# Optimization experiments

Measured on AMD Instinct MI355X. Metric: run time of the kernel, lower is better.

The kernel has to match this reference:

```python
import jax, jax.numpy as jnp
import numpy as np

D_MODEL = 1024
NUM_HEADS = 16
D_K = D_MODEL // NUM_HEADS
THETA = 10000.0
BATCH = 2
SEQ = 2048


def _trunc_normal(key, shape, std):
    # approximate trunc_normal init; exact init distribution is irrelevant for correctness
    return jnp.clip(jax.random.normal(key, shape) * std, -3.0 * std, 3.0 * std)


def setup_inputs() -> dict:
    key = jax.random.key(0)
    ks = jax.random.split(key, 6)
    std = np.sqrt(2.0 / (D_MODEL + D_MODEL)).astype(np.float32)
    x = jax.random.normal(ks[0], (BATCH, SEQ, D_MODEL), dtype=jnp.float32)
    token_positions = jnp.tile(jnp.arange(SEQ, dtype=jnp.int32), (BATCH, 1))
    wq = _trunc_normal(ks[1], (D_MODEL, D_MODEL), std)  # (out, in)
    wk = _trunc_normal(ks[2], (D_MODEL, D_MODEL), std)
    wv = _trunc_normal(ks[3], (D_MODEL, D_MODEL), std)
    wo = _trunc_normal(ks[4], (D_MODEL, D_MODEL), std)
    return {"in_features": x, "wq": wq, "wk": wk, "wv": wv, "wo": wo,
            "token_positions": token_positions}


def _apply_rope(x, token_positions):
    # x: (B, H, S, d_k); token_positions: (B, S)
    half = D_K // 2
    inv_freq = 1.0 / (THETA ** (2.0 * jnp.arange(half, dtype=jnp.float32) / D_K))
    ang = token_positions.astype(jnp.float32)[..., None] * inv_freq  # (B, S, half)
    cos = jnp.cos(ang)[:, None, :, :]  # (B, 1, S, half) broadcast over heads
    sin = jnp.sin(ang)[:, None, :, :]
    x_even = x[..., 0::2]
    x_odd = x[..., 1::2]
    rot_even = x_even * cos - x_odd * sin
    rot_odd = x_even * sin + x_odd * cos
    return jnp.stack([rot_even, rot_odd], axis=-1).reshape(x.shape)


def reference(in_features, wq, wk, wv, wo, token_positions):
    B, S, _ = in_features.shape
    # bias-free linear: weight is (out, in)
    q = jnp.einsum('bsi,oi->bso', in_features, wq)
    k = jnp.einsum('bsi,oi->bso', in_features, wk)
    v = jnp.einsum('bsi,oi->bso', in_features, wv)
    # split heads: (B, H, S, d_k)
    def split(t):
        return t.reshape(B, S, NUM_HEADS, D_K).transpose(0, 2, 1, 3)
    qh, kh, vh = split(q), split(k), split(v)
    qh = _apply_rope(qh, token_positions)
    kh = _apply_rope(kh, token_positions)
    scale = 1.0 / jnp.sqrt(jnp.float32(D_K))
    logits = jnp.einsum('bhqd,bhkd->bhqk', qh, kh) * scale  # (B, H, S, S)
    causal = jnp.tril(jnp.ones((S, S), dtype=bool))
    logits = jnp.where(causal, logits, -jnp.inf)
    weights = jax.nn.softmax(logits, axis=-1)
    out = jnp.einsum('bhqk,bhkd->bhqd', weights, vh)  # (B, H, S, d_k)
    out = out.transpose(0, 2, 1, 3).reshape(B, S, D_MODEL)
    return jnp.einsum('bsi,oi->bso', out, wo)
```

## Files before the change

kernel.cpp:

```cpp
#include <hip/hip_runtime.h>
#include <hip/hip_bf16.h>
#include <math.h>

#define D_MODEL 1024
#define NUM_HEADS 16
#define DK 64
#define BATCH 2
#define SEQ 2048
#define NROWS (BATCH * SEQ)

typedef __bf16 bf16x8 __attribute__((ext_vector_type(8)));
typedef __bf16 bf16x4 __attribute__((ext_vector_type(4)));
typedef float f32x4 __attribute__((ext_vector_type(4)));

#define GLOAD_LDS16(g, l)                                          \
  __builtin_amdgcn_global_load_lds(                                \
      (const __attribute__((address_space(1))) void*)(g),          \
      (__attribute__((address_space(3))) void*)(l), 16, 0, 0)

#define LDS_FENCE() asm volatile("s_waitcnt lgkmcnt(0)" ::: "memory")

__global__ void cvt_all_kernel(const float* __restrict__ x,
                               const float* __restrict__ wq,
                               const float* __restrict__ wk,
                               const float* __restrict__ wv,
                               const float* __restrict__ wo,
                               __hip_bfloat16* __restrict__ xb,
                               __hip_bfloat16* __restrict__ wqkvb,
                               __hip_bfloat16* __restrict__ wob) {
  int t = blockIdx.x * 256 + threadIdx.x;
  const float* src;
  __hip_bfloat16* dst;
  int off;
  if (t < 1048576) {
    src = x; dst = xb; off = t;
  } else {
    int u = t - 1048576;
    int w = u >> 18;
    off = u & 262143;
    src = (w == 0) ? wq : (w == 1) ? wk : (w == 2) ? wv : wo;
    dst = (w < 3) ? (wqkvb + (size_t)w * 1048576) : wob;
  }
  float4 v = reinterpret_cast<const float4*>(src)[off];
  union { __hip_bfloat16 h[4]; uint2 u; } tmp;
  tmp.h[0] = __float2bfloat16(v.x);
  tmp.h[1] = __float2bfloat16(v.y);
  tmp.h[2] = __float2bfloat16(v.z);
  tmp.h[3] = __float2bfloat16(v.w);
  reinterpret_cast<uint2*>(dst)[off] = tmp.u;
}

__global__ __launch_bounds__(256)
void gemm_qkv_kernel(const __hip_bfloat16* __restrict__ A,
                     const __hip_bfloat16* __restrict__ W,
                     __hip_bfloat16* __restrict__ O0,
                     __hip_bfloat16* __restrict__ O1,
                     __hip_bfloat16* __restrict__ Vt) {
  __shared__ __hip_bfloat16 smem[2][2][128 * 32];
#define sAg(b) (smem[0][b])
#define sBg(b) (smem[1][b])
  const int tid = threadIdx.x;
  const int wave = tid >> 6, lane = tid & 63, quad = lane >> 4, l16 = lane & 15;
  const int wm = (wave >> 1) * 64, wn = (wave & 1) * 64;
  const int bm = blockIdx.x * 128;
  const int bnG = blockIdx.y * 128;
  const int which = blockIdx.y >> 3;
  const int ocol = bnG & 1023;
  const int srow = lane >> 2, scol = (lane & 3) * 8;

#pragma unroll
  for (int c = 0; c < 2; ++c) {
    int ch = wave + c * 4;
    GLOAD_LDS16(&A[(size_t)(bm + ch * 16 + srow) * D_MODEL + scol], &sAg(0)[ch * 512]);
    GLOAD_LDS16(&W[(size_t)(bnG + ch * 16 + srow) * D_MODEL + scol], &sBg(0)[ch * 512]);
  }

  f32x4 acc[4][4] = {};
  for (int it = 0; it < 32; ++it) {
    __syncthreads();
    if (it + 1 < 32) {
      const int k0 = (it + 1) * 32, nb = (it + 1) & 1;
#pragma unroll
      for (int c = 0; c < 2; ++c) {
        int ch = wave + c * 4;
        GLOAD_LDS16(&A[(size_t)(bm + ch * 16 + srow) * D_MODEL + k0 + scol],
                    &sAg(nb)[ch * 512]);
        GLOAD_LDS16(&W[(size_t)(bnG + ch * 16 + srow) * D_MODEL + k0 + scol],
                    &sBg(nb)[ch * 512]);
      }
    }
    const int cb = it & 1;
    bf16x8 af[4], bfb[4];
#pragma unroll
    for (int i = 0; i < 4; ++i)
      af[i] = *reinterpret_cast<bf16x8*>(&sAg(cb)[(wm + i * 16 + l16) * 32 + quad * 8]);
#pragma unroll
    for (int j = 0; j < 4; ++j)
      bfb[j] = *reinterpret_cast<bf16x8*>(&sBg(cb)[(wn + j * 16 + l16) * 32 + quad * 8]);
#pragma unroll
    for (int i = 0; i < 4; ++i)
#pragma unroll
      for (int j = 0; j < 4; ++j)
        acc[i][j] = __builtin_amdgcn_mfma_f32_16x16x32_bf16(af[i], bfb[j], acc[i][j], 0, 0, 0);
  }

  if (which < 2) {
    __hip_bfloat16* O = (which == 0) ? O0 : O1;
#pragma unroll
    for (int i = 0; i < 4; ++i)
#pragma unroll
      for (int j = 0; j < 4; ++j)
#pragma unroll
        for (int r = 0; r < 4; ++r) {
          int row = bm + wm + i * 16 + quad * 4 + r;
          int col = ocol + wn + j * 16 + l16;
          O[(size_t)row * D_MODEL + col] = __float2bfloat16(acc[i][j][r]);
        }
  } else {
    __syncthreads();
    __hip_bfloat16* tr = &smem[0][0][0];
#pragma unroll
    for (int i = 0; i < 4; ++i)
#pragma unroll
      for (int j = 0; j < 4; ++j) {
        int c = wn + j * 16 + l16;
        int r = wm + i * 16 + quad * 4;
        bf16x4 pk;
#pragma unroll
        for (int rr = 0; rr < 4; ++rr) pk[rr] = (__bf16)acc[i][j][rr];
        int g = (r >> 3) ^ (c & 15);
        *reinterpret_cast<bf16x4*>(&tr[c * 128 + g * 8 + (r & 7)]) = pk;
      }
    __syncthreads();
    int c = tid >> 1;
    int vcol = ocol + c;
    int hh = vcol >> 6, dd = vcol & 63;
    int bb = bm >> 11, s0 = (bm & 2047) + (tid & 1) * 64;
    __hip_bfloat16* dst = Vt + ((size_t)(bb * 16 + hh) * 64 + dd) * 2048 + s0;
    int gbase = (tid & 1) * 8;
#pragma unroll
    for (int k = 0; k < 8; ++k) {
      int g = (gbase + k) ^ (c & 15);
      *reinterpret_cast<bf16x8*>(&dst[k * 8]) =
          *reinterpret_cast<bf16x8*>(&tr[c * 128 + g * 8]);
    }
  }
#undef sAg
#undef sBg
}

__global__ __launch_bounds__(256)
void gemm_out_kernel(const __hip_bfloat16* __restrict__ A,
                     const __hip_bfloat16* __restrict__ W,
                     float* __restrict__ O) {
  __shared__ __hip_bfloat16 sA[2][64 * 32];
  __shared__ __hip_bfloat16 sB[2][128 * 32];
  const int tid = threadIdx.x;
  const int wave = tid >> 6, lane = tid & 63, quad = lane >> 4, l16 = lane & 15;
  const int mh = (wave >> 1) * 32, nh = (wave & 1) * 64;
  const int bm = blockIdx.x * 64, bn = blockIdx.y * 128;
  const int srow = lane >> 2, scol = (lane & 3) * 8;

  GLOAD_LDS16(&A[(size_t)(bm + wave * 16 + srow) * D_MODEL + scol], &sA[0][wave * 512]);
#pragma unroll
  for (int c = 0; c < 2; ++c) {
    int ch = wave + c * 4;
    GLOAD_LDS16(&W[(size_t)(bn + ch * 16 + srow) * D_MODEL + scol], &sB[0][ch * 512]);
  }

  f32x4 acc[2][4] = {};
  for (int it = 0; it < 32; ++it) {
    __syncthreads();
    if (it + 1 < 32) {
      const int k0 = (it + 1) * 32, nb = (it + 1) & 1;
      GLOAD_LDS16(&A[(size_t)(bm + wave * 16 + srow) * D_MODEL + k0 + scol],
                  &sA[nb][wave * 512]);
#pragma unroll
      for (int c = 0; c < 2; ++c) {
        int ch = wave + c * 4;
        GLOAD_LDS16(&W[(size_t)(bn + ch * 16 + srow) * D_MODEL + k0 + scol],
                    &sB[nb][ch * 512]);
      }
    }
    const int cb = it & 1;
    bf16x8 af[2], bfb[4];
#pragma unroll
    for (int i = 0; i < 2; ++i)
      af[i] = *reinterpret_cast<bf16x8*>(&sA[cb][(mh + i * 16 + l16) * 32 + quad * 8]);
#pragma unroll
    for (int j = 0; j < 4; ++j)
      bfb[j] = *reinterpret_cast<bf16x8*>(&sB[cb][(nh + j * 16 + l16) * 32 + quad * 8]);
#pragma unroll
    for (int i = 0; i < 2; ++i)
#pragma unroll
      for (int j = 0; j < 4; ++j)
        acc[i][j] = __builtin_amdgcn_mfma_f32_16x16x32_bf16(af[i], bfb[j], acc[i][j], 0, 0, 0);
  }

#pragma unroll
  for (int i = 0; i < 2; ++i)
#pragma unroll
    for (int j = 0; j < 4; ++j)
#pragma unroll
      for (int r = 0; r < 4; ++r) {
        int row = bm + mh + i * 16 + quad * 4 + r;
        int col = bn + nh + j * 16 + l16;
        O[(size_t)row * D_MODEL + col] = acc[i][j][r];
      }
}

__global__ void rope_kernel(__hip_bfloat16* __restrict__ Q,
                            __hip_bfloat16* __restrict__ K,
                            const int* __restrict__ pos) {
  constexpr float QS = 0.18033688011112042f;
  int t = blockIdx.x * 256 + threadIdx.x;
  int row = t >> 7;
  int c = t & 127;
  int h = c >> 3, co = (c & 7) * 8;
  float ps = (float)pos[row];
  size_t off = (size_t)row * D_MODEL + h * DK + co;
  bf16x8 q = *reinterpret_cast<const bf16x8*>(&Q[off]);
  bf16x8 k = *reinterpret_cast<const bf16x8*>(&K[off]);
#pragma unroll
  for (int j = 0; j < 4; ++j) {
    float p = (float)((co >> 1) + j);
    float ang = ps * exp2f(-p * 0.41524101186091903f);
    float cs = cosf(ang), sn = sinf(ang);
    float qe = (float)q[2 * j], qo = (float)q[2 * j + 1];
    q[2 * j]     = (__bf16)((qe * cs - qo * sn) * QS);
    q[2 * j + 1] = (__bf16)((qe * sn + qo * cs) * QS);
    float ke = (float)k[2 * j], ko = (float)k[2 * j + 1];
    k[2 * j]     = (__bf16)(ke * cs - ko * sn);
    k[2 * j + 1] = (__bf16)(ke * sn + ko * cs);
  }
  *reinterpret_cast<bf16x8*>(&Q[off]) = q;
  *reinterpret_cast<bf16x8*>(&K[off]) = k;
}

__global__ __launch_bounds__(256)
void attn_kernel(const __hip_bfloat16* __restrict__ Q,
                 const __hip_bfloat16* __restrict__ K,
                 const __hip_bfloat16* __restrict__ Vt,
                 __hip_bfloat16* __restrict__ Ao) {
  __shared__ __hip_bfloat16 sK[2][64 * 64];
  __shared__ __hip_bfloat16 sVt[2][64 * 64];
  __shared__ __hip_bfloat16 sPt[4][16 * 64];
  const int tid = threadIdx.x;
  const int wave = tid >> 6, lane = tid & 63, quad = lane >> 4, l16 = lane & 15;
  const int idx = blockIdx.x;
  const int bh = idx & 31;
  const int half = (idx >> 5) & 1;
  const int pi = idx >> 6;
  const int qlo = pi, qhi = 15 - pi;
  const int h = bh & 15, b = bh >> 4;
  const int ho = h * DK;
  const size_t rowbase = (size_t)b * SEQ;
  const int jL = half * 4 + wave, jU = 7 - jL;
  const int sbs[2] = {qlo * 128 + jL * 16, qhi * 128 + jU * 16};
  const int nt = ((qhi * 128 + (7 - half * 4) * 16 + 15) >> 6) + 1;
  const __hip_bfloat16* Kbase = K + rowbase * D_MODEL + ho;
  const __hip_bfloat16* Vtbase = Vt + (size_t)(b * 16 + h) * 64 * 2048;

  bf16x8 aq[2][2];
#pragma unroll
  for (int s = 0; s < 2; ++s)
#pragma unroll
    for (int kk = 0; kk < 2; ++kk)
      aq[s][kk] = *reinterpret_cast<const bf16x8*>(
          &Q[(rowbase + sbs[s] + l16) * D_MODEL + ho + kk * 32 + quad * 8]);

  f32x4 o_acc[2][4] = {};
  float l_run[2] = {0.f, 0.f};

  const int srow = tid >> 2, sc = (tid & 3) * 16;
  const int ga = (tid & 3) * 2;
  const int sga = (ga ^ (srow & 7)) * 8, sgb = ((ga + 1) ^ (srow & 7)) * 8;

  {
    bf16x8 k0 = *reinterpret_cast<const bf16x8*>(&Kbase[(size_t)srow * D_MODEL + sc]);
    bf16x8 k1 = *reinterpret_cast<const bf16x8*>(&Kbase[(size_t)srow * D_MODEL + sc + 8]);
    bf16x8 v0 = *reinterpret_cast<const bf16x8*>(&Vtbase[(size_t)srow * 2048 + sc]);
    bf16x8 v1 = *reinterpret_cast<const bf16x8*>(&Vtbase[(size_t)srow * 2048 + sc + 8]);
    *reinterpret_cast<bf16x8*>(&sK[0][srow * 64 + sga]) = k0;
    *reinterpret_cast<bf16x8*>(&sK[0][srow * 64 + sgb]) = k1;
    *reinterpret_cast<bf16x8*>(&sVt[0][srow * 64 + sga]) = v0;
    *reinterpret_cast<bf16x8*>(&sVt[0][srow * 64 + sgb]) = v1;
  }

  for (int t = 0; t < nt; ++t) {
    __syncthreads();
    const int buf = t & 1;
    const bool hn = (t + 1) < nt;
    bf16x8 kn0, kn1, vn0, vn1;
    if (hn) {
      const int kvn = (t + 1) * 64;
      kn0 = *reinterpret_cast<const bf16x8*>(
          &Kbase[(size_t)(kvn + srow) * D_MODEL + sc]);
      kn1 = *reinterpret_cast<const bf16x8*>(
          &Kbase[(size_t)(kvn + srow) * D_MODEL + sc + 8]);
      vn0 = *reinterpret_cast<const bf16x8*>(
          &Vtbase[(size_t)srow * 2048 + kvn + sc]);
      vn1 = *reinterpret_cast<const bf16x8*>(
          &Vtbase[(size_t)srow * 2048 + kvn + sc + 8]);
    }

    const int kv0 = t * 64;
    if (kv0 <= sbs[1] + 15) {
      bf16x8 ak[2][4], bv[2][4];
#pragma unroll
      for (int kk = 0; kk < 2; ++kk)
#pragma unroll
        for (int j = 0; j < 4; ++j) {
          int go = ((4 * kk + quad) ^ (l16 & 7)) * 8;
          ak[kk][j] = *reinterpret_cast<bf16x8*>(&sK[buf][(j * 16 + l16) * 64 + go]);
          bv[kk][j] = *reinterpret_cast<bf16x8*>(&sVt[buf][(j * 16 + l16) * 64 + go]);
        }

#pragma unroll
      for (int s = 0; s < 2; ++s) {
        const int sb = sbs[s];
        if (kv0 > sb + 15) continue;
        f32x4 sv[4] = {};
#pragma unroll
        for (int kk = 0; kk < 2; ++kk)
#pragma unroll
          for (int j = 0; j < 4; ++j)
            sv[j] = __builtin_amdgcn_mfma_f32_16x16x32_bf16(ak[kk][j], aq[s][kk],
                                                            sv[j], 0, 0, 0);
        if (kv0 + 63 > sb) {
#pragma unroll
          for (int j = 0; j < 4; ++j)
#pragma unroll
            for (int r = 0; r < 4; ++r)
              if (kv0 + j * 16 + quad * 4 + r > sb + l16) sv[j][r] = -INFINITY;
        }
        float ls = 0.f;
#pragma unroll
        for (int j = 0; j < 4; ++j) {
          bf16x4 pk;
#pragma unroll
          for (int r = 0; r < 4; ++r) {
            float p = __builtin_amdgcn_exp2f(sv[j][r]);
            ls += p;
            pk[r] = (__bf16)p;
          }
          int wgr = (2 * j + (quad >> 1)) ^ (l16 & 7);
          *reinterpret_cast<bf16x4*>(
              &sPt[wave][l16 * 64 + wgr * 8 + (quad & 1) * 4]) = pk;
        }
        l_run[s] += ls;
        LDS_FENCE();
#pragma unroll
        for (int kk = 0; kk < 2; ++kk) {
          int rgr = (4 * kk + quad) ^ (l16 & 7);
          bf16x8 ap = *reinterpret_cast<bf16x8*>(&sPt[wave][l16 * 64 + rgr * 8]);
#pragma unroll
          for (int jd = 0; jd < 4; ++jd)
            o_acc[s][jd] = __builtin_amdgcn_mfma_f32_16x16x32_bf16(
                ap, bv[kk][jd], o_acc[s][jd], 0, 0, 0);
        }
      }
    }

    if (hn) {
      const int nb = buf ^ 1;
      *reinterpret_cast<bf16x8*>(&sK[nb][srow * 64 + sga]) = kn0;
      *reinterpret_cast<bf16x8*>(&sK[nb][srow * 64 + sgb]) = kn1;
      *reinterpret_cast<bf16x8*>(&sVt[nb][srow * 64 + sga]) = vn0;
      *reinterpret_cast<bf16x8*>(&sVt[nb][srow * 64 + sgb]) = vn1;
    }
  }

#pragma unroll
  for (int s = 0; s < 2; ++s) {
    float l = l_run[s];
    l += __shfl_xor(l, 16);
    l += __shfl_xor(l, 32);
    __hip_bfloat16* Aobase = Ao + (rowbase + sbs[s]) * D_MODEL + ho;
#pragma unroll
    for (int r = 0; r < 4; ++r) {
      float linv = 1.0f / __shfl(l, quad * 4 + r);
#pragma unroll
      for (int jd = 0; jd < 4; ++jd)
        Aobase[(size_t)(quad * 4 + r) * D_MODEL + jd * 16 + l16] =
            __float2bfloat16(o_acc[s][jd][r] * linv);
    }
  }
}

extern "C" void kernel_launch(void* const* d_in, const int* in_sizes, int n_in,
                              void* d_out, int out_size, void* d_ws, size_t ws_size,
                              hipStream_t stream) {
  const float* x = (const float*)d_in[0];
  const float* wq = (const float*)d_in[1];
  const float* wk = (const float*)d_in[2];
  const float* wv = (const float*)d_in[3];
  const float* wo = (const float*)d_in[4];
  const int* tpos = (const int*)d_in[5];
  float* out = (float*)d_out;
  char* ws = (char*)d_ws;

  __hip_bfloat16* xb    = (__hip_bfloat16*)(ws);
  __hip_bfloat16* wqkvb = (__hip_bfloat16*)(ws + (size_t)(8)  * 1048576);
  __hip_bfloat16* wob   = (__hip_bfloat16*)(ws + (size_t)(14) * 1048576);
  __hip_bfloat16* Qb    = (__hip_bfloat16*)(ws + (size_t)(16) * 1048576);
  __hip_bfloat16* Kb    = (__hip_bfloat16*)(ws + (size_t)(24) * 1048576);
  __hip_bfloat16* Vtb   = (__hip_bfloat16*)(ws + (size_t)(32) * 1048576);
  __hip_bfloat16* Aob   = xb;

  cvt_all_kernel<<<8192, 256, 0, stream>>>(x, wq, wk, wv, wo, xb, wqkvb, wob);

  gemm_qkv_kernel<<<dim3(32, 24), 256, 0, stream>>>(xb, wqkvb, Qb, Kb, Vtb);

  rope_kernel<<<2048, 256, 0, stream>>>(Qb, Kb, tpos);

  attn_kernel<<<512, 256, 0, stream>>>(Qb, Kb, Vtb, Aob);

  gemm_out_kernel<<<dim3(64, 8), 256, 0, stream>>>(Aob, wob, out);
}
```

Baseline: 182.4 us.

## Fuse RoPE into QKV GEMM epilogue and shrink output GEMM tiles

Applies the rotary embedding and the Q scaling directly in the QKV GEMM epilogue, pairing even and odd columns with a lane shuffle and using fast sincos. This removes the separate rope kernel launch and its full read-modify-write pass over Q and K. The output projection GEMM also switches from 64x128 to 64x64 tiles, doubling the grid to 1024 blocks for better CU occupancy at the cost of more redundant A loads. __sincosf is less accurate than cosf/sinf at the large angles produced by positions up to 2047.

```diff
diff --git a/kernel.cpp b/kernel.cpp
--- a/kernel.cpp
+++ b/kernel.cpp
@@ -53,9 +53,11 @@
 __global__ __launch_bounds__(256)
 void gemm_qkv_kernel(const __hip_bfloat16* __restrict__ A,
                      const __hip_bfloat16* __restrict__ W,
+                     const int* __restrict__ tpos,
                      __hip_bfloat16* __restrict__ O0,
                      __hip_bfloat16* __restrict__ O1,
                      __hip_bfloat16* __restrict__ Vt) {
+  constexpr float QS = 0.18033688011112042f;
   __shared__ __hip_bfloat16 smem[2][2][128 * 32];
 #define sAg(b) (smem[0][b])
 #define sBg(b) (smem[1][b])
@@ -106,16 +108,31 @@
 
   if (which < 2) {
     __hip_bfloat16* O = (which == 0) ? O0 : O1;
+    const float scale = (which == 0) ? QS : 1.0f;
+    const float sgn = (l16 & 1) ? 1.0f : -1.0f;
+    float invf[4];
+#pragma unroll
+    for (int j = 0; j < 4; ++j) {
+      int p = ((ocol + wn + j * 16 + l16) & 63) >> 1;
+      invf[j] = exp2f(-(float)p * 0.41524101186091903f);
+    }
 #pragma unroll
     for (int i = 0; i < 4; ++i)
 #pragma unroll
-      for (int j = 0; j < 4; ++j)
-#pragma unroll
-        for (int r = 0; r < 4; ++r) {
-          int row = bm + wm + i * 16 + quad * 4 + r;
+      for (int r = 0; r < 4; ++r) {
+        int row = bm + wm + i * 16 + quad * 4 + r;
+        float pos = (float)tpos[row];
+#pragma unroll
+        for (int j = 0; j < 4; ++j) {
+          float v = acc[i][j][r];
+          float partner = __shfl_xor(v, 1);
+          float sn, cs;
+          __sincosf(pos * invf[j], &sn, &cs);
+          float rot = (v * cs + sgn * partner * sn) * scale;
           int col = ocol + wn + j * 16 + l16;
-          O[(size_t)row * D_MODEL + col] = __float2bfloat16(acc[i][j][r]);
-        }
+          O[(size_t)row * D_MODEL + col] = __float2bfloat16(rot);
+        }
+      }
   } else {
     __syncthreads();
     __hip_bfloat16* tr = &smem[0][0][0];
@@ -154,87 +171,51 @@
                      const __hip_bfloat16* __restrict__ W,
                      float* __restrict__ O) {
   __shared__ __hip_bfloat16 sA[2][64 * 32];
-  __shared__ __hip_bfloat16 sB[2][128 * 32];
+  __shared__ __hip_bfloat16 sB[2][64 * 32];
   const int tid = threadIdx.x;
   const int wave = tid >> 6, lane = tid & 63, quad = lane >> 4, l16 = lane & 15;
-  const int mh = (wave >> 1) * 32, nh = (wave & 1) * 64;
-  const int bm = blockIdx.x * 64, bn = blockIdx.y * 128;
+  const int mh = (wave >> 1) * 32, nh = (wave & 1) * 32;
+  const int bm = blockIdx.x * 64, bn = blockIdx.y * 64;
   const int srow = lane >> 2, scol = (lane & 3) * 8;
 
   GLOAD_LDS16(&A[(size_t)(bm + wave * 16 + srow) * D_MODEL + scol], &sA[0][wave * 512]);
-#pragma unroll
-  for (int c = 0; c < 2; ++c) {
-    int ch = wave + c * 4;
-    GLOAD_LDS16(&W[(size_t)(bn + ch * 16 + srow) * D_MODEL + scol], &sB[0][ch * 512]);
-  }
-
-  f32x4 acc[2][4] = {};
+  GLOAD_LDS16(&W[(size_t)(bn + wave * 16 + srow) * D_MODEL + scol], &sB[0][wave * 512]);
+
+  f32x4 acc[2][2] = {};
   for (int it = 0; it < 32; ++it) {
     __syncthreads();
     if (it + 1 < 32) {
       const int k0 = (it + 1) * 32, nb = (it + 1) & 1;
       GLOAD_LDS16(&A[(size_t)(bm + wave * 16 + srow) * D_MODEL + k0 + scol],
                   &sA[nb][wave * 512]);
-#pragma unroll
-      for (int c = 0; c < 2; ++c) {
-        int ch = wave + c * 4;
-        GLOAD_LDS16(&W[(size_t)(bn + ch * 16 + srow) * D_MODEL + k0 + scol],
-                    &sB[nb][ch * 512]);
-      }
+      GLOAD_LDS16(&W[(size_t)(bn + wave * 16 + srow) * D_MODEL + k0 + scol],
+                  &sB[nb][wave * 512]);
     }
     const int cb = it & 1;
-    bf16x8 af[2], bfb[4];
+    bf16x8 af[2], bfb[2];
 #pragma unroll
     for (int i = 0; i < 2; ++i)
       af[i] = *reinterpret_cast<bf16x8*>(&sA[cb][(mh + i * 16 + l16) * 32 + quad * 8]);
 #pragma unroll
-    for (int j = 0; j < 4; ++j)
+    for (int j = 0; j < 2; ++j)
       bfb[j] = *reinterpret_cast<bf16x8*>(&sB[cb][(nh + j * 16 + l16) * 32 + quad * 8]);
 #pragma unroll
     for (int i = 0; i < 2; ++i)
 #pragma unroll
-      for (int j = 0; j < 4; ++j)
+      for (int j = 0; j < 2; ++j)
         acc[i][j] = __builtin_amdgcn_mfma_f32_16x16x32_bf16(af[i], bfb[j], acc[i][j], 0, 0, 0);
   }
 
 #pragma unroll
   for (int i = 0; i < 2; ++i)
 #pragma unroll
-    for (int j = 0; j < 4; ++j)
+    for (int j = 0; j < 2; ++j)
 #pragma unroll
       for (int r = 0; r < 4; ++r) {
         int row = bm + mh + i * 16 + quad * 4 + r;
         int col = bn + nh + j * 16 + l16;
         O[(size_t)row * D_MODEL + col] = acc[i][j][r];
       }
-}
-
-__global__ void rope_kernel(__hip_bfloat16* __restrict__ Q,
-                            __hip_bfloat16* __restrict__ K,
-                            const int* __restrict__ pos) {
-  constexpr float QS = 0.18033688011112042f;
-  int t = blockIdx.x * 256 + threadIdx.x;
-  int row = t >> 7;
-  int c = t & 127;
-  int h = c >> 3, co = (c & 7) * 8;
-  float ps = (float)pos[row];
-  size_t off = (size_t)row * D_MODEL + h * DK + co;
-  bf16x8 q = *reinterpret_cast<const bf16x8*>(&Q[off]);
-  bf16x8 k = *reinterpret_cast<const bf16x8*>(&K[off]);
-#pragma unroll
-  for (int j = 0; j < 4; ++j) {
-    float p = (float)((co >> 1) + j);
-    float ang = ps * exp2f(-p * 0.41524101186091903f);
-    float cs = cosf(ang), sn = sinf(ang);
-    float qe = (float)q[2 * j], qo = (float)q[2 * j + 1];
-    q[2 * j]     = (__bf16)((qe * cs - qo * sn) * QS);
-    q[2 * j + 1] = (__bf16)((qe * sn + qo * cs) * QS);
-    float ke = (float)k[2 * j], ko = (float)k[2 * j + 1];
-    k[2 * j]     = (__bf16)(ke * cs - ko * sn);
-    k[2 * j + 1] = (__bf16)(ke * sn + ko * cs);
-  }
-  *reinterpret_cast<bf16x8*>(&Q[off]) = q;
-  *reinterpret_cast<bf16x8*>(&K[off]) = k;
 }
 
 __global__ __launch_bounds__(256)
@@ -410,11 +391,9 @@
 
   cvt_all_kernel<<<8192, 256, 0, stream>>>(x, wq, wk, wv, wo, xb, wqkvb, wob);
 
-  gemm_qkv_kernel<<<dim3(32, 24), 256, 0, stream>>>(xb, wqkvb, Qb, Kb, Vtb);
-
-  rope_kernel<<<2048, 256, 0, stream>>>(Qb, Kb, tpos);
+  gemm_qkv_kernel<<<dim3(32, 24), 256, 0, stream>>>(xb, wqkvb, tpos, Qb, Kb, Vtb);
 
   attn_kernel<<<512, 256, 0, stream>>>(Qb, Kb, Vtb, Aob);
 
-  gemm_out_kernel<<<dim3(64, 8), 256, 0, stream>>>(Aob, wob, out);
-}
+  gemm_out_kernel<<<dim3(64, 16), 256, 0, stream>>>(Aob, wob, out);
+}
```

Result: faster. 175.4 us (-3.8%).
